# Kernel optimization log

Measured on AMD Instinct MI355X. Metric: run time of the kernel, lower is better.

## Reference

```python
import jax, jax.numpy as jnp
import numpy as np

HID, H, P = 1024, 16, 50  # hid_dim, n_heads, max_relative_position
DH = HID // H


def _rel_idx(len_q, len_k):
    # [Lq, Lk] clipped relative-distance indices into the (2P+1)-row table
    d = jnp.arange(len_k)[None, :] - jnp.arange(len_q)[:, None]
    return jnp.clip(d, -P, P) + P


def setup_inputs() -> dict:
    key = jax.random.key(0)
    ks = jax.random.split(key, 13)
    L, B = 2048, 2
    s = 0.02
    return {
        "query": jax.random.normal(ks[0], (L, B, HID), jnp.float32),
        "key": jax.random.normal(ks[1], (L, B, HID), jnp.float32),
        "value": jax.random.normal(ks[2], (L, B, HID), jnp.float32),
        "Wq": jax.random.normal(ks[3], (HID, HID), jnp.float32) * s,
        "bq": jax.random.normal(ks[4], (HID,), jnp.float32) * s,
        "Wk": jax.random.normal(ks[5], (HID, HID), jnp.float32) * s,
        "bk": jax.random.normal(ks[6], (HID,), jnp.float32) * s,
        "Wv": jax.random.normal(ks[7], (HID, HID), jnp.float32) * s,
        "bv": jax.random.normal(ks[8], (HID,), jnp.float32) * s,
        "Wo": jax.random.normal(ks[9], (HID, HID), jnp.float32) * s,
        "bo": jax.random.normal(ks[10], (HID,), jnp.float32) * s,
        "rel_k": jax.random.normal(ks[11], (2 * P + 1, DH), jnp.float32) * s,
        "rel_v": jax.random.normal(ks[12], (2 * P + 1, DH), jnp.float32) * s,
    }


def reference(query, key, value, Wq, bq, Wk, bk, Wv, bv, Wo, bo, rel_k, rel_v):
    # inputs are seq-first [L, B, hid]; torch code transposes to batch-first
    q = jnp.swapaxes(query, 0, 1)  # [B, Lq, hid]
    k = jnp.swapaxes(key, 0, 1)
    v = jnp.swapaxes(value, 0, 1)
    B, Lq, _ = q.shape
    Lk = k.shape[1]

    q = q @ Wq.T + bq
    k = k @ Wk.T + bk
    v = v @ Wv.T + bv

    # split heads: [B, H, L, DH]
    qh = q.reshape(B, Lq, H, DH).transpose(0, 2, 1, 3)
    kh = k.reshape(B, Lk, H, DH).transpose(0, 2, 1, 3)
    vh = v.reshape(B, Lk, H, DH).transpose(0, 2, 1, 3)

    idx = _rel_idx(Lq, Lk)
    Rk = rel_k[idx]  # [Lq, Lk, DH]
    Rv = rel_v[idx]  # [Lq, Lk, DH]

    attn1 = jnp.einsum('bhqd,bhkd->bhqk', qh, kh)
    attn2 = jnp.einsum('bhqd,qkd->bhqk', qh, Rk)
    scale = jnp.asarray(np.sqrt(DH), qh.dtype)
    attn = jax.nn.softmax((attn1 + attn2) / scale, axis=-1)  # dropout p=0 -> identity

    w1 = jnp.einsum('bhqk,bhkd->bhqd', attn, vh)
    w2 = jnp.einsum('bhqk,qkd->bhqd', attn, Rv)
    x = (w1 + w2).transpose(0, 2, 1, 3).reshape(B, Lq, HID)
    x = x @ Wo.T + bo
    return jnp.swapaxes(x, 0, 1)  # [Lq, B, hid]
```

## Files before the change

### kernel.cpp

```cpp
#include <hip/hip_runtime.h>


#define LSEQ 2048
#define HIDDIM 1024
#define NH 16
#define DHD 64
#define NREL 101
#define PMAX 50
#define SCL 0.18033688011112042f

typedef __attribute__((ext_vector_type(8))) __bf16 bf16x8;
typedef __attribute__((ext_vector_type(4))) float f32x4;

#define MFMA(A, B, C) __builtin_amdgcn_mfma_f32_16x16x32_bf16(A, B, C, 0, 0, 0)
#define LDS_FENCE() asm volatile("s_waitcnt lgkmcnt(0)" ::: "memory")

__device__ __forceinline__ unsigned short f2bf(float f) {
  unsigned int u = __builtin_bit_cast(unsigned int, f);
  u += 0x7fffu + ((u >> 16) & 1u);
  return (unsigned short)(u >> 16);
}
__device__ __forceinline__ float bflo(unsigned int u) { return __builtin_bit_cast(float, u << 16); }

__device__ __forceinline__ unsigned cvtpk(float lo, float hi) {
  unsigned r;
  asm("v_cvt_pk_bf16_f32 %0, %1, %2" : "=v"(r) : "v"(lo), "v"(hi));
  return r;
}
__device__ __forceinline__ float pklo(unsigned pk) { return __builtin_bit_cast(float, pk << 16); }
__device__ __forceinline__ float pkhi(unsigned pk) { return __builtin_bit_cast(float, pk & 0xffff0000u); }

__device__ __forceinline__ uint4 pack8(float4 f0, float4 f1) {
  uint4 o;
  o.x = (unsigned)f2bf(f0.x) | ((unsigned)f2bf(f0.y) << 16);
  o.y = (unsigned)f2bf(f0.z) | ((unsigned)f2bf(f0.w) << 16);
  o.z = (unsigned)f2bf(f1.x) | ((unsigned)f2bf(f1.y) << 16);
  o.w = (unsigned)f2bf(f1.z) | ((unsigned)f2bf(f1.w) << 16);
  return o;
}

__device__ __forceinline__ void gload16(const unsigned short* g, unsigned short* l) {
  __builtin_amdgcn_global_load_lds(
      (const __attribute__((address_space(1))) unsigned int*)g,
      (__attribute__((address_space(3))) unsigned int*)l, 16, 0, 0);
}

__global__ void cast_w4(const float* __restrict__ s0, const float* __restrict__ s1,
                        const float* __restrict__ s2, const float* __restrict__ s3,
                        unsigned short* __restrict__ dst) {
  const int e = (blockIdx.x * 256 + threadIdx.x) * 8;
  const int g = e >> 20;
  const float* s = (g == 0) ? s0 : (g == 1) ? s1 : (g == 2) ? s2 : s3;
  const int o = e & 0xFFFFF;
  const float4 f0 = *(const float4*)(s + o);
  const float4 f1 = *(const float4*)(s + o + 4);
  *(uint4*)(dst + e) = pack8(f0, f1);
}

__global__ void cast_x3(const float* __restrict__ q, const float* __restrict__ k,
                        const float* __restrict__ v,
                        unsigned short* __restrict__ dq, unsigned short* __restrict__ dk,
                        unsigned short* __restrict__ dv) {
  const int gid = blockIdx.x * 256 + threadIdx.x;
  const int segi = gid >> 19;
  const int e = (gid & 0x7FFFF) * 8;
  const float* s = (segi == 0) ? q : (segi == 1) ? k : v;
  unsigned short* dst = (segi == 0) ? dq : (segi == 1) ? dk : dv;
  const int m = e >> 10, kk = e & 1023;
  const int b = m >> 11, l = m & 2047;
  const float* sp = s + (size_t)((l << 1) + b) * HIDDIM + kk;
  const float4 f0 = *(const float4*)sp;
  const float4 f1 = *(const float4*)(sp + 4);
  *(uint4*)(dst + e) = pack8(f0, f1);
}

__global__ void cast_rel(const float* __restrict__ rk, const float* __restrict__ rv,
                         unsigned short* __restrict__ dk, unsigned short* __restrict__ dv) {
  const int e = blockIdx.x * 256 + threadIdx.x;
  if (e < 112 * 64) {
    dk[e] = (e < NREL * 64) ? f2bf(rk[e]) : (unsigned short)0;
  } else {
    const int e2 = e - 112 * 64;
    if (e2 >= 64 * 128) return;
    const int d = e2 >> 7, j = e2 & 127;
    dv[e2] = (j < NREL) ? f2bf(rv[j * DHD + d]) : (unsigned short)0;
  }
}

__global__ __launch_bounds__(256, 3) void gemm_qkv(
    const unsigned short* __restrict__ Xq, const unsigned short* __restrict__ Xk,
    const unsigned short* __restrict__ Xv, const unsigned short* __restrict__ Wcat,
    const float* __restrict__ bq, const float* __restrict__ bk, const float* __restrict__ bv,
    unsigned short* __restrict__ Qb, unsigned short* __restrict__ Kb,
    unsigned short* __restrict__ Vgt) {
  __shared__ __align__(16) unsigned short SH[17408];
  unsigned short* LA = SH;
  unsigned short* LB = SH + 8192;

  const int tid = threadIdx.x;
  const int seg = blockIdx.x >> 8;
  const int t = blockIdx.x & 255;
  const int m0 = (t >> 3) * 128, n0 = (t & 7) * 128;

  const unsigned short* A = (seg == 0) ? Xq : (seg == 1) ? Xk : Xv;
  const unsigned short* W = Wcat + ((size_t)seg << 20);
  const float* bias = (seg == 0) ? bq : (seg == 1) ? bk : bv;

  const int lane = tid & 63, w = tid >> 6;
  const int c = lane & 15, quad = lane >> 4;

  const int srow = w * 32 + (lane >> 3);
  const int scol = ((lane & 7) ^ (lane >> 3)) << 3;
  const unsigned short* pA = A + (size_t)(m0 + srow) * 1024 + scol;
  const unsigned short* pW = W + (size_t)(n0 + srow) * 1024 + scol;
  unsigned short* lA = LA + w * 2048;
  unsigned short* lB = LB + w * 2048;

  const int wr = w >> 1, wc = w & 1;
  const int cx = (c & 7) << 3;

  f32x4 acc[4][4] = {};

  for (int k0 = 0; k0 < 1024; k0 += 64) {
#pragma unroll
    for (int i = 0; i < 4; i++) {
      gload16(pA + k0 + i * 8192, lA + i * 512);
      gload16(pW + k0 + i * 8192, lB + i * 512);
    }
    __syncthreads();
#pragma unroll
    for (int ks = 0; ks < 2; ks++) {
      bf16x8 af[4], bfr[4];
#pragma unroll
      for (int f = 0; f < 4; f++) {
        af[f]  = *(const bf16x8*)&LA[(wr * 64 + f * 16 + c) * 64 + ((ks * 32 + quad * 8) ^ cx)];
        bfr[f] = *(const bf16x8*)&LB[(wc * 64 + f * 16 + c) * 64 + ((ks * 32 + quad * 8) ^ cx)];
      }
#pragma unroll
      for (int i = 0; i < 4; i++)
#pragma unroll
        for (int j = 0; j < 4; j++)
          acc[i][j] = MFMA(af[i], bfr[j], acc[i][j]);
    }
    __syncthreads();
  }

  const int b = m0 >> 11, l0 = m0 & 2047;
  const int h0 = n0 >> 6;
  if (seg < 2) {
    unsigned short* out = seg ? Kb : Qb;
#pragma unroll
    for (int i = 0; i < 4; i++)
#pragma unroll
      for (int j = 0; j < 4; j++) {
        const int nl = wc * 64 + j * 16 + c;
        const float bv_ = bias[n0 + nl];
        const int h = h0 + (nl >> 6), d = nl & 63;
#pragma unroll
        for (int r = 0; r < 4; r++) {
          const int l = l0 + wr * 64 + i * 16 + quad * 4 + r;
          out[((size_t)((b * NH + h) * LSEQ + l) << 6) + d] = f2bf(acc[i][j][r] + bv_);
        }
      }
  } else {
    unsigned short* Ct = SH;
#pragma unroll
    for (int i = 0; i < 4; i++)
#pragma unroll
      for (int j = 0; j < 4; j++) {
        const int nl = wc * 64 + j * 16 + c;
        const float bv_ = bias[n0 + nl];
#pragma unroll
        for (int r = 0; r < 4; r++) {
          const int ml = wr * 64 + i * 16 + quad * 4 + r;
          Ct[nl * 136 + ml] = f2bf(acc[i][j][r] + bv_);
        }
      }
    __syncthreads();
    const int dr = tid >> 1, lc = (tid & 1) * 64;
    const int h = h0 + (dr >> 6), dd = dr & 63;
    unsigned short* dst = Vgt + ((size_t)((b * NH + h) * 64 + dd)) * LSEQ + l0 + lc;
    const unsigned short* src = Ct + dr * 136 + lc;
#pragma unroll
    for (int u = 0; u < 8; u++)
      *(uint4*)(dst + u * 8) = *(const uint4*)(src + u * 8);
  }
}

__global__ __launch_bounds__(256, 3) void gemm_out(
    const unsigned short* __restrict__ A,
    const unsigned short* __restrict__ W,
    const float* __restrict__ bias,
    float* __restrict__ outF) {
  __shared__ __align__(16) unsigned short SH[16384];
  unsigned short* LA = SH;
  unsigned short* LB = SH + 8192;

  const int tid = threadIdx.x;
  const int t = blockIdx.x;
  const int m0 = (t >> 3) * 128, n0 = (t & 7) * 128;

  const int lane = tid & 63, w = tid >> 6;
  const int c = lane & 15, quad = lane >> 4;

  const int srow = w * 32 + (lane >> 3);
  const int scol = ((lane & 7) ^ (lane >> 3)) << 3;
  const unsigned short* pA = A + (size_t)(m0 + srow) * 1024 + scol;
  const unsigned short* pW = W + (size_t)(n0 + srow) * 1024 + scol;
  unsigned short* lA = LA + w * 2048;
  unsigned short* lB = LB + w * 2048;

  const int wr = w >> 1, wc = w & 1;
  const int cx = (c & 7) << 3;

  f32x4 acc[4][4] = {};

  for (int k0 = 0; k0 < 1024; k0 += 64) {
#pragma unroll
    for (int i = 0; i < 4; i++) {
      gload16(pA + k0 + i * 8192, lA + i * 512);
      gload16(pW + k0 + i * 8192, lB + i * 512);
    }
    __syncthreads();
#pragma unroll
    for (int ks = 0; ks < 2; ks++) {
      bf16x8 af[4], bfr[4];
#pragma unroll
      for (int f = 0; f < 4; f++) {
        af[f]  = *(const bf16x8*)&LA[(wr * 64 + f * 16 + c) * 64 + ((ks * 32 + quad * 8) ^ cx)];
        bfr[f] = *(const bf16x8*)&LB[(wc * 64 + f * 16 + c) * 64 + ((ks * 32 + quad * 8) ^ cx)];
      }
#pragma unroll
      for (int i = 0; i < 4; i++)
#pragma unroll
        for (int j = 0; j < 4; j++)
          acc[i][j] = MFMA(af[i], bfr[j], acc[i][j]);
    }
    __syncthreads();
  }

  const int b = m0 >> 11, l0 = m0 & 2047;
#pragma unroll
  for (int i = 0; i < 4; i++)
#pragma unroll
    for (int j = 0; j < 4; j++) {
      const int n = n0 + wc * 64 + j * 16 + c;
      const float bv_ = bias[n];
#pragma unroll
      for (int r = 0; r < 4; r++) {
        const int l = l0 + wr * 64 + i * 16 + quad * 4 + r;
        outF[(size_t)((l << 1) + b) * HIDDIM + n] = acc[i][j][r] + bv_;
      }
    }
}

#define KT 32
__global__ __launch_bounds__(256, 4) void attn_mfma(
    const unsigned short* __restrict__ Qb,
    const unsigned short* __restrict__ Kb,
    const unsigned short* __restrict__ Vgt,
    const unsigned short* __restrict__ RKb,
    const unsigned short* __restrict__ RVb,
    unsigned short* __restrict__ outB) {
  __shared__ __align__(16) unsigned short SH[20480];
  unsigned short* Kst = SH;

  const int tid = threadIdx.x;
  const int xcd = blockIdx.x & 7, slot = blockIdx.x >> 3;
  const int bh = (slot >> 5) * 8 + xcd;
  const int q0 = (slot & 31) * 64;

  const int lane = tid & 63, wq = tid >> 6;
  const int c = lane & 15, quad = lane >> 4;
  unsigned short* Ptw = SH + 4608 + wq * 640;
  unsigned short* Tb  = SH + 7168 + wq * 1664;
  unsigned short* SrS = SH + 13824 + wq * 1664;

  const size_t base = (size_t)bh * (LSEQ * DHD);
  const unsigned short* Qp = Qb + base;
  const unsigned short* Kp = Kb + base;
  const unsigned short* Vp = Vgt + base;

  const int qrow_w = q0 + wq * 16;

  {
    uint4 z = {0u, 0u, 0u, 0u};
    uint4* tz = (uint4*)(SH + 7168);
    for (int e = tid; e < 832; e += 256) tz[e] = z;
  }

  const bf16x8 aq0 = *(const bf16x8*)&Qp[(size_t)(qrow_w + c) * DHD + quad * 8];
  const bf16x8 aq1 = *(const bf16x8*)&Qp[(size_t)(qrow_w + c) * DHD + 32 + quad * 8];

#pragma unroll
  for (int jt = 0; jt < 7; jt++) {
    const bf16x8 rk0 = *(const bf16x8*)&RKb[(jt * 16 + c) * DHD + quad * 8];
    const bf16x8 rk1 = *(const bf16x8*)&RKb[(jt * 16 + c) * DHD + 32 + quad * 8];
    f32x4 s4 = {};
    s4 = MFMA(rk0, aq0, s4);
    s4 = MFMA(rk1, aq1, s4);
    const int jb = jt * 16 + quad * 4;
    const unsigned p01 = cvtpk(s4[0], s4[1]);
    const unsigned p23 = cvtpk(s4[2], s4[3]);
    if (jb <= 102)     *(unsigned*)&SrS[c * 104 + jb] = p01;
    if (jb + 2 <= 102) *(unsigned*)&SrS[c * 104 + jb + 2] = p23;
  }

  const int strow = tid >> 3, stcol = (tid & 7) * 8;
  {
    uint4 k0r = *(const uint4*)&Kp[(size_t)strow * DHD + stcol];
    *(uint4*)&Kst[strow * 72 + stcol] = k0r;
  }
  __syncthreads();

  const float srvlo = bflo((unsigned)SrS[c * 104 + 0]);
  const float srvhi = bflo((unsigned)SrS[c * 104 + 100]);

  float lows = 0.f, highs = 0.f, mids = 0.f;
  f32x4 Od[4] = {};

  for (int it = 0; it < 64; ++it) {
    const int k0 = it * KT;
    const int cur = (it & 1) * 2304;
    uint4 kreg;
    if (it < 63) kreg = *(const uint4*)&Kp[(size_t)(k0 + KT + strow) * DHD + stcol];
    bf16x8 vf[4];
#pragma unroll
    for (int t = 0; t < 4; t++)
      vf[t] = *(const bf16x8*)&Vp[(size_t)(t * 16 + c) * LSEQ + k0 + quad * 8];

    const bf16x8 ka00 = *(const bf16x8*)&Kst[cur + c * 72 + quad * 8];
    const bf16x8 ka01 = *(const bf16x8*)&Kst[cur + c * 72 + 32 + quad * 8];
    const bf16x8 ka10 = *(const bf16x8*)&Kst[cur + (16 + c) * 72 + quad * 8];
    const bf16x8 ka11 = *(const bf16x8*)&Kst[cur + (16 + c) * 72 + 32 + quad * 8];
    f32x4 s0 = {}, s1 = {};
    s0 = MFMA(ka00, aq0, s0);
    s0 = MFMA(ka01, aq1, s0);
    s1 = MFMA(ka10, aq0, s1);
    s1 = MFMA(ka11, aq1, s1);

    const int mode = (k0 + KT - 1 <= qrow_w - 50) ? 0 : (k0 >= qrow_w + 65) ? 2 : 1;

    unsigned pkA0, pkA1, pkB0, pkB1;
    if (mode != 1) {
      const float srv = (mode == 0) ? srvlo : srvhi;
      const float e0 = exp2f((s0[0] + srv) * SCL);
      const float e1 = exp2f((s0[1] + srv) * SCL);
      const float e2 = exp2f((s0[2] + srv) * SCL);
      const float e3 = exp2f((s0[3] + srv) * SCL);
      const float e4 = exp2f((s1[0] + srv) * SCL);
      const float e5 = exp2f((s1[1] + srv) * SCL);
      const float e6 = exp2f((s1[2] + srv) * SCL);
      const float e7 = exp2f((s1[3] + srv) * SCL);
      pkA0 = cvtpk(e0, e1); pkA1 = cvtpk(e2, e3);
      pkB0 = cvtpk(e4, e5); pkB1 = cvtpk(e6, e7);
      const float sq = ((pklo(pkA0) + pkhi(pkA0)) + (pklo(pkA1) + pkhi(pkA1)))
                     + ((pklo(pkB0) + pkhi(pkB0)) + (pklo(pkB1) + pkhi(pkB1)));
      if (mode == 0) lows += sq; else highs += sq;
    } else {
      const int kb0 = k0 + quad * 4 - (qrow_w + c) + 50;
      float ee[8]; int jj[8];
#pragma unroll
      for (int r = 0; r < 4; r++) {
        int j0 = kb0 + r;       j0 = j0 < 0 ? 0 : (j0 > 100 ? 100 : j0);
        int j1 = kb0 + 16 + r;  j1 = j1 < 0 ? 0 : (j1 > 100 ? 100 : j1);
        jj[r] = j0; jj[4 + r] = j1;
        const float sv0 = bflo((unsigned)SrS[c * 104 + j0]);
        const float sv1 = bflo((unsigned)SrS[c * 104 + j1]);
        ee[r]     = exp2f((s0[r] + sv0) * SCL);
        ee[4 + r] = exp2f((s1[r] + sv1) * SCL);
      }
      pkA0 = cvtpk(ee[0], ee[1]); pkA1 = cvtpk(ee[2], ee[3]);
      pkB0 = cvtpk(ee[4], ee[5]); pkB1 = cvtpk(ee[6], ee[7]);
      const unsigned pks[4] = {pkA0, pkA1, pkB0, pkB1};
#pragma unroll
      for (int i = 0; i < 4; i++) {
        const unsigned pk = pks[i];
        const float plo = pklo(pk), phi = pkhi(pk);
        const int jl = jj[2 * i], jh = jj[2 * i + 1];
        if (jl == 0) lows += plo;
        else if (jl == 100) highs += plo;
        else { mids += plo; Tb[c * 104 + jl] = (unsigned short)pk; }
        if (jh == 0) lows += phi;
        else if (jh == 100) highs += phi;
        else { mids += phi; Tb[c * 104 + jh] = (unsigned short)(pk >> 16); }
      }
    }

    uint2 w0; w0.x = pkA0; w0.y = pkA1;
    uint2 w1; w1.x = pkB0; w1.y = pkB1;
    *(uint2*)&Ptw[c * 40 + quad * 4] = w0;
    *(uint2*)&Ptw[c * 40 + 16 + quad * 4] = w1;
    LDS_FENCE();
    const bf16x8 ap = *(const bf16x8*)&Ptw[c * 40 + quad * 8];
#pragma unroll
    for (int t = 0; t < 4; t++)
      Od[t] = MFMA(ap, vf[t], Od[t]);

    if (it < 63) *(uint4*)&Kst[(cur ^ 2304) + strow * 72 + stcol] = kreg;
    __syncthreads();
  }

#pragma unroll
  for (int m = 16; m < 64; m <<= 1) {
    lows  += __shfl_xor(lows,  m, 64);
    highs += __shfl_xor(highs, m, 64);
    mids  += __shfl_xor(mids,  m, 64);
  }
  const float rsum = (lows + highs) + mids;
  if (lane < 16) {
    Tb[c * 104 + 0]   = f2bf(lows);
    Tb[c * 104 + 100] = f2bf(highs);
  }
  LDS_FENCE();

#pragma unroll
  for (int kc = 0; kc < 4; kc++) {
    uint4 zz = {0u, 0u, 0u, 0u};
    bf16x8 at = __builtin_bit_cast(bf16x8, zz);
    if (kc < 3 || quad == 0) at = *(const bf16x8*)&Tb[c * 104 + kc * 32 + quad * 8];
#pragma unroll
    for (int t = 0; t < 4; t++) {
      const bf16x8 bv = *(const bf16x8*)&RVb[(t * 16 + c) * 128 + kc * 32 + quad * 8];
      Od[t] = MFMA(at, bv, Od[t]);
    }
  }

  const int b = bh >> 4, h = bh & 15;
#pragma unroll
  for (int r = 0; r < 4; r++) {
    const float rs = __shfl(rsum, quad * 4 + r, 64);
    const float inv = 1.f / rs;
    const int qg = qrow_w + quad * 4 + r;
    unsigned short* op = outB + (size_t)(b * LSEQ + qg) * HIDDIM + h * DHD + c;
#pragma unroll
    for (int t = 0; t < 4; t++) op[t * 16] = f2bf(Od[t][r] * inv);
  }
}

extern "C" void kernel_launch(void* const* d_in, const int* in_sizes, int n_in,
                              void* d_out, int out_size, void* d_ws, size_t ws_size,
                              hipStream_t stream) {
  const float* query = (const float*)d_in[0];
  const float* key   = (const float*)d_in[1];
  const float* value = (const float*)d_in[2];
  const float* Wq = (const float*)d_in[3];  const float* bq = (const float*)d_in[4];
  const float* Wk = (const float*)d_in[5];  const float* bk = (const float*)d_in[6];
  const float* Wv = (const float*)d_in[7];  const float* bv = (const float*)d_in[8];
  const float* Wo = (const float*)d_in[9];  const float* bo = (const float*)d_in[10];
  const float* relk = (const float*)d_in[11];
  const float* relv = (const float*)d_in[12];
  float* out = (float*)d_out;

  char* w = (char*)d_ws;
  const size_t MB = 1ull << 20;
  unsigned short* Wcat = (unsigned short*)(w + 0 * MB);
  unsigned short* Wob  = (unsigned short*)(w + 6 * MB);
  unsigned short* Xq   = (unsigned short*)(w + 8 * MB);
  unsigned short* Qb   = (unsigned short*)(w + 16 * MB);
  unsigned short* Kb   = (unsigned short*)(w + 24 * MB);
  unsigned short* Vgt  = (unsigned short*)(w + 32 * MB);
  unsigned short* AOb  = Xq;
  unsigned short* RKb  = Wcat;
  unsigned short* RVb  = (unsigned short*)(w + 2 * MB);
  unsigned short* Xk = (unsigned short*)out;
  unsigned short* Xv = (unsigned short*)out + (4u << 20);

  cast_w4<<<2048, 256, 0, stream>>>(Wq, Wk, Wv, Wo, Wcat);
  cast_x3<<<6144, 256, 0, stream>>>(query, key, value, Xq, Xk, Xv);
  gemm_qkv<<<768, 256, 0, stream>>>(Xq, Xk, Xv, Wcat, bq, bk, bv, Qb, Kb, Vgt);
  cast_rel<<<60, 256, 0, stream>>>(relk, relv, RKb, RVb);
  attn_mfma<<<1024, 256, 0, stream>>>(Qb, Kb, Vgt, RKb, RVb, AOb);
  gemm_out<<<256, 256, 0, stream>>>(AOb, Wob, bo, out);
}
```

Baseline: 325.9 us.

## Merge cast kernels, stage Q/K epilogue through LDS, shrink output GEMM tile

Measured after the change: 325.1 us. About the same (-0.3%).

```diff
diff --git a/kernel.cpp b/kernel.cpp
--- a/kernel.cpp
+++ b/kernel.cpp
@@ -45,33 +45,35 @@
       (__attribute__((address_space(3))) unsigned int*)l, 16, 0, 0);
 }
 
-__global__ void cast_w4(const float* __restrict__ s0, const float* __restrict__ s1,
-                        const float* __restrict__ s2, const float* __restrict__ s3,
-                        unsigned short* __restrict__ dst) {
-  const int e = (blockIdx.x * 256 + threadIdx.x) * 8;
-  const int g = e >> 20;
-  const float* s = (g == 0) ? s0 : (g == 1) ? s1 : (g == 2) ? s2 : s3;
-  const int o = e & 0xFFFFF;
-  const float4 f0 = *(const float4*)(s + o);
-  const float4 f1 = *(const float4*)(s + o + 4);
-  *(uint4*)(dst + e) = pack8(f0, f1);
-}
-
-__global__ void cast_x3(const float* __restrict__ q, const float* __restrict__ k,
-                        const float* __restrict__ v,
+__global__ void cast_wx(const float* __restrict__ w0, const float* __restrict__ w1,
+                        const float* __restrict__ w2, const float* __restrict__ w3,
+                        const float* __restrict__ xq, const float* __restrict__ xk,
+                        const float* __restrict__ xv,
+                        unsigned short* __restrict__ Wcat,
                         unsigned short* __restrict__ dq, unsigned short* __restrict__ dk,
                         unsigned short* __restrict__ dv) {
-  const int gid = blockIdx.x * 256 + threadIdx.x;
-  const int segi = gid >> 19;
-  const int e = (gid & 0x7FFFF) * 8;
-  const float* s = (segi == 0) ? q : (segi == 1) ? k : v;
-  unsigned short* dst = (segi == 0) ? dq : (segi == 1) ? dk : dv;
-  const int m = e >> 10, kk = e & 1023;
-  const int b = m >> 11, l = m & 2047;
-  const float* sp = s + (size_t)((l << 1) + b) * HIDDIM + kk;
-  const float4 f0 = *(const float4*)sp;
-  const float4 f1 = *(const float4*)(sp + 4);
-  *(uint4*)(dst + e) = pack8(f0, f1);
+  const int bid = blockIdx.x;
+  if (bid < 2048) {
+    const int e = (bid * 256 + threadIdx.x) * 8;
+    const int g = e >> 20;
+    const float* s = (g == 0) ? w0 : (g == 1) ? w1 : (g == 2) ? w2 : w3;
+    const int o = e & 0xFFFFF;
+    const float4 f0 = *(const float4*)(s + o);
+    const float4 f1 = *(const float4*)(s + o + 4);
+    *(uint4*)(Wcat + e) = pack8(f0, f1);
+  } else {
+    const int gid = (bid - 2048) * 256 + threadIdx.x;
+    const int segi = gid >> 19;
+    const int e = (gid & 0x7FFFF) * 8;
+    const float* s = (segi == 0) ? xq : (segi == 1) ? xk : xv;
+    unsigned short* dst = (segi == 0) ? dq : (segi == 1) ? dk : dv;
+    const int m = e >> 10, kk = e & 1023;
+    const int b = m >> 11, l = m & 2047;
+    const float* sp = s + (size_t)((l << 1) + b) * HIDDIM + kk;
+    const float4 f0 = *(const float4*)sp;
+    const float4 f1 = *(const float4*)(sp + 4);
+    *(uint4*)(dst + e) = pack8(f0, f1);
+  }
 }
 
 __global__ void cast_rel(const float* __restrict__ rk, const float* __restrict__ rv,
@@ -148,20 +150,27 @@
   const int b = m0 >> 11, l0 = m0 & 2047;
   const int h0 = n0 >> 6;
   if (seg < 2) {
-    unsigned short* out = seg ? Kb : Qb;
+    unsigned short* Ct = SH;
 #pragma unroll
     for (int i = 0; i < 4; i++)
 #pragma unroll
       for (int j = 0; j < 4; j++) {
         const int nl = wc * 64 + j * 16 + c;
         const float bv_ = bias[n0 + nl];
-        const int h = h0 + (nl >> 6), d = nl & 63;
 #pragma unroll
         for (int r = 0; r < 4; r++) {
-          const int l = l0 + wr * 64 + i * 16 + quad * 4 + r;
-          out[((size_t)((b * NH + h) * LSEQ + l) << 6) + d] = f2bf(acc[i][j][r] + bv_);
+          const int ml = wr * 64 + i * 16 + quad * 4 + r;
+          Ct[ml * 136 + nl] = f2bf(acc[i][j][r] + bv_);
         }
       }
+    __syncthreads();
+    unsigned short* out = seg ? Kb : Qb;
+    const int ll = tid >> 1, hh = tid & 1;
+    unsigned short* dst = out + ((size_t)((b * NH + h0 + hh) * LSEQ + l0 + ll)) * 64;
+    const unsigned short* src = Ct + ll * 136 + hh * 64;
+#pragma unroll
+    for (int u = 0; u < 8; u++)
+      *(uint4*)(dst + u * 8) = *(const uint4*)(src + u * 8);
   } else {
     unsigned short* Ct = SH;
 #pragma unroll
@@ -187,54 +196,55 @@
   }
 }
 
-__global__ __launch_bounds__(256, 3) void gemm_out(
+__global__ __launch_bounds__(256, 2) void gemm_out(
     const unsigned short* __restrict__ A,
     const unsigned short* __restrict__ W,
     const float* __restrict__ bias,
     float* __restrict__ outF) {
-  __shared__ __align__(16) unsigned short SH[16384];
+  __shared__ __align__(16) unsigned short SH[12288];
   unsigned short* LA = SH;
-  unsigned short* LB = SH + 8192;
+  unsigned short* LB = SH + 4096;
 
   const int tid = threadIdx.x;
   const int t = blockIdx.x;
-  const int m0 = (t >> 3) * 128, n0 = (t & 7) * 128;
+  const int m0 = (t >> 3) * 64, n0 = (t & 7) * 128;
 
   const int lane = tid & 63, w = tid >> 6;
   const int c = lane & 15, quad = lane >> 4;
 
-  const int srow = w * 32 + (lane >> 3);
-  const int scol = ((lane & 7) ^ (lane >> 3)) << 3;
-  const unsigned short* pA = A + (size_t)(m0 + srow) * 1024 + scol;
-  const unsigned short* pW = W + (size_t)(n0 + srow) * 1024 + scol;
-  unsigned short* lA = LA + w * 2048;
+  const int sr8 = lane >> 3;
+  const int scol = ((lane & 7) ^ sr8) << 3;
+  const unsigned short* pA = A + (size_t)(m0 + w * 16 + sr8) * 1024 + scol;
+  const unsigned short* pW = W + (size_t)(n0 + w * 32 + sr8) * 1024 + scol;
+  unsigned short* lA = LA + w * 1024;
   unsigned short* lB = LB + w * 2048;
 
-  const int wr = w >> 1, wc = w & 1;
   const int cx = (c & 7) << 3;
 
-  f32x4 acc[4][4] = {};
+  f32x4 acc[4][2] = {};
 
   for (int k0 = 0; k0 < 1024; k0 += 64) {
 #pragma unroll
-    for (int i = 0; i < 4; i++) {
+    for (int i = 0; i < 2; i++)
       gload16(pA + k0 + i * 8192, lA + i * 512);
+#pragma unroll
+    for (int i = 0; i < 4; i++)
       gload16(pW + k0 + i * 8192, lB + i * 512);
-    }
     __syncthreads();
 #pragma unroll
     for (int ks = 0; ks < 2; ks++) {
-      bf16x8 af[4], bfr[4];
-#pragma unroll
-      for (int f = 0; f < 4; f++) {
-        af[f]  = *(const bf16x8*)&LA[(wr * 64 + f * 16 + c) * 64 + ((ks * 32 + quad * 8) ^ cx)];
-        bfr[f] = *(const bf16x8*)&LB[(wc * 64 + f * 16 + c) * 64 + ((ks * 32 + quad * 8) ^ cx)];
-      }
+      bf16x8 af[4], bf2[2];
+#pragma unroll
+      for (int f = 0; f < 4; f++)
+        af[f] = *(const bf16x8*)&LA[(f * 16 + c) * 64 + ((ks * 32 + quad * 8) ^ cx)];
+#pragma unroll
+      for (int f = 0; f < 2; f++)
+        bf2[f] = *(const bf16x8*)&LB[(w * 32 + f * 16 + c) * 64 + ((ks * 32 + quad * 8) ^ cx)];
 #pragma unroll
       for (int i = 0; i < 4; i++)
 #pragma unroll
-        for (int j = 0; j < 4; j++)
-          acc[i][j] = MFMA(af[i], bfr[j], acc[i][j]);
+        for (int j = 0; j < 2; j++)
+          acc[i][j] = MFMA(af[i], bf2[j], acc[i][j]);
     }
     __syncthreads();
   }
@@ -243,12 +253,12 @@
 #pragma unroll
   for (int i = 0; i < 4; i++)
 #pragma unroll
-    for (int j = 0; j < 4; j++) {
-      const int n = n0 + wc * 64 + j * 16 + c;
+    for (int j = 0; j < 2; j++) {
+      const int n = n0 + w * 32 + j * 16 + c;
       const float bv_ = bias[n];
 #pragma unroll
       for (int r = 0; r < 4; r++) {
-        const int l = l0 + wr * 64 + i * 16 + quad * 4 + r;
+        const int l = l0 + i * 16 + quad * 4 + r;
         outF[(size_t)((l << 1) + b) * HIDDIM + n] = acc[i][j][r] + bv_;
       }
     }
@@ -466,10 +476,9 @@
   unsigned short* Xk = (unsigned short*)out;
   unsigned short* Xv = (unsigned short*)out + (4u << 20);
 
-  cast_w4<<<2048, 256, 0, stream>>>(Wq, Wk, Wv, Wo, Wcat);
-  cast_x3<<<6144, 256, 0, stream>>>(query, key, value, Xq, Xk, Xv);
+  cast_wx<<<8192, 256, 0, stream>>>(Wq, Wk, Wv, Wo, query, key, value, Wcat, Xq, Xk, Xv);
   gemm_qkv<<<768, 256, 0, stream>>>(Xq, Xk, Xv, Wcat, bq, bk, bv, Qb, Kb, Vgt);
   cast_rel<<<60, 256, 0, stream>>>(relk, relv, RKb, RVb);
   attn_mfma<<<1024, 256, 0, stream>>>(Qb, Kb, Vgt, RKb, RVb, AOb);
-  gemm_out<<<256, 256, 0, stream>>>(AOb, Wob, bo, out);
-}
+  gemm_out<<<512, 256, 0, stream>>>(AOb, Wob, bo, out);
+}
```
